# Optimization experiments

Measured on AMD Instinct MI355X. Metric: run time of the kernel, lower is better.

Reference implementation:

```python
import jax, jax.numpy as jnp
import numpy as np

N = 50000   # nodes
E = 800000  # edges
IN = 256    # input feature dim
H = 4       # heads (per layer)
D = 64      # num_hidden per head
C = 16      # n_clusters
NEG = 0.2   # leaky_relu negative slope


def _gat_conv(x, W, attn_l, attn_r, src, dst):
    """DGL GATConv (no residual, no dropout at eval), activation=elu.
    x: [N, F_in], W: [F_in, H*D], attn_l/attn_r: [H, D]. Returns [N, H, D]."""
    feat = (x @ W).reshape(N, H, D)                      # [N,H,D]
    el = jnp.sum(feat * attn_l, axis=-1)                 # [N,H]
    er = jnp.sum(feat * attn_r, axis=-1)                 # [N,H]
    e = jax.nn.leaky_relu(el[src] + er[dst], NEG)        # [E,H]
    # numerically stable segment softmax over incoming edges of each dst node
    emax = jax.ops.segment_max(e, dst, num_segments=N)   # [N,H]
    emax = jnp.where(jnp.isfinite(emax), emax, 0.0)
    ee = jnp.exp(e - emax[dst])                          # [E,H]
    denom = jax.ops.segment_sum(ee, dst, num_segments=N) # [N,H]
    a = ee / jnp.maximum(denom[dst], 1e-9)               # [E,H]
    msg = feat[src] * a[:, :, None]                      # [E,H,D]
    rst = jax.ops.segment_sum(msg, dst, num_segments=N)  # [N,H,D]
    return jax.nn.elu(rst)


def setup_inputs() -> dict:
    key = jax.random.key(0)
    ks = jax.random.split(key, 12)
    def w(k, shape, fan):
        return jax.random.normal(k, shape, jnp.float32) * np.float32(1.0 / np.sqrt(fan))
    return {
        "x": jax.random.normal(ks[0], (N, IN), jnp.float32),
        "src": jax.random.randint(ks[1], (E,), 0, N, jnp.int32),
        "dst": jax.random.randint(ks[2], (E,), 0, N, jnp.int32),
        "W0": w(ks[3], (IN, H * D), IN),
        "al0": w(ks[4], (H, D), D),
        "ar0": w(ks[5], (H, D), D),
        "W1": w(ks[6], (H * D, H * D), H * D),
        "al1": w(ks[7], (H, D), D),
        "ar1": w(ks[8], (H, D), D),
        "Wc": w(ks[9], (D, C), D),
        "bc": jnp.zeros((C,), jnp.float32),
    }


def reference(x, src, dst, W0, al0, ar0, W1, al1, ar1, Wc, bc):
    h = _gat_conv(x, W0, al0, ar0, src, dst)              # [N,H,D]
    h = _gat_conv(h.reshape(N, H * D), W1, al1, ar1, src, dst)
    heads = jnp.transpose(h, (1, 0, 2))                   # [H,N,D]
    # original bug: same cluster layer (index num_layers-1) used for every head
    cs = jax.nn.softmax(jnp.einsum("hnd,dc->hnc", heads, Wc) + bc, axis=-1)  # [H,N,C]
    # pack (heads, cs) into one array along last dim for a single output
    return jnp.concatenate([heads, cs], axis=-1)          # [H,N,D+C]
```

## Files before the change

### kernel.cpp

```cpp
#include <hip/hip_runtime.h>
#include <hip/hip_bf16.h>
#include <math.h>

#define N_NODES 50000
#define N_EDGES 800000
#define NH 4
#define ND 64
#define NF 256
#define NC 16
#define NEG_SLOPE 0.2f
#define NSLICE 4
#define SLICE_W 64

typedef __attribute__((ext_vector_type(8))) short bf16x8;
typedef __attribute__((ext_vector_type(4))) float f32x4;

__device__ __forceinline__ float elu_f(float x) {
    return x > 0.f ? x : (__expf(x) - 1.f);
}

__device__ __forceinline__ ushort bf16_rne(float f) {
    union { float f; unsigned u; } v; v.f = f;
    unsigned u = v.u;
    u += 0x7fffu + ((u >> 16) & 1u);
    return (ushort)(u >> 16);
}

__device__ __forceinline__ float bf2f(ushort u) {
    return __uint_as_float(((unsigned)u) << 16);
}

__global__ __launch_bounds__(256) void cast_bf16_kernel(const float* __restrict__ in,
                                                        ushort* __restrict__ out, int n8) {
    int i = blockIdx.x * 256 + threadIdx.x;
    if (i >= n8) return;
    float4 a = *(const float4*)(in + i * 8);
    float4 b = *(const float4*)(in + i * 8 + 4);
    ushort o[8] = {bf16_rne(a.x), bf16_rne(a.y), bf16_rne(a.z), bf16_rne(a.w),
                   bf16_rne(b.x), bf16_rne(b.y), bf16_rne(b.z), bf16_rne(b.w)};
    *(bf16x8*)(out + i * 8) = *(bf16x8*)o;
}

__global__ __launch_bounds__(256) void castWt_kernel(const float* __restrict__ W0,
                                                     const float* __restrict__ W1,
                                                     ushort* __restrict__ Wt0,
                                                     ushort* __restrict__ Wt1) {
    const float* W = (blockIdx.x < 256) ? W0 : W1;
    ushort* Wt = (blockIdx.x < 256) ? Wt0 : Wt1;
    int n = blockIdx.x & 255;
    int k = threadIdx.x;
    Wt[n * 256 + k] = bf16_rne(W[k * 256 + n]);
}

__global__ __launch_bounds__(256) void gemm_bf16(const ushort* __restrict__ A,
                                                 const ushort* __restrict__ Bt,
                                                 ushort* __restrict__ Cs,
                                                 const float* __restrict__ al,
                                                 const float* __restrict__ ar,
                                                 float* __restrict__ el,
                                                 float* __restrict__ er, int M) {
    __shared__ __align__(16) ushort As[128 * 64];
    __shared__ __align__(16) ushort Bs[128 * 64];
    const int t = threadIdx.x;
    const int l = t & 63;
    const int w = t >> 6;
    const int wm = (w >> 1) * 64, wn = (w & 1) * 64;
    const int m0 = blockIdx.x * 128, n0 = blockIdx.y * 128;
    const int lr = l & 15, lk = l >> 4;

    f32x4 acc[4][4] = {};
    const int sr = t >> 3;
    const int sc = t & 7;
    const int scw = sc ^ (sr & 7);

    for (int k0 = 0; k0 < 256; k0 += 64) {
        #pragma unroll
        for (int q = 0; q < 4; ++q) {
            int row = q * 32 + sr;
            int ga = min(m0 + row, M - 1);
            bf16x8 va = *(const bf16x8*)(A + (size_t)ga * 256 + k0 + sc * 8);
            *(bf16x8*)(&As[row * 64 + scw * 8]) = va;
            bf16x8 vb = *(const bf16x8*)(Bt + (size_t)(n0 + row) * 256 + k0 + sc * 8);
            *(bf16x8*)(&Bs[row * 64 + scw * 8]) = vb;
        }
        __syncthreads();
        #pragma unroll
        for (int kk = 0; kk < 2; ++kk) {
            bf16x8 af[4], bfr[4];
            #pragma unroll
            for (int mi = 0; mi < 4; ++mi) {
                int row = wm + mi * 16 + lr;
                int kb = kk * 4 + lk;
                af[mi] = *(const bf16x8*)(&As[row * 64 + (kb ^ (row & 7)) * 8]);
            }
            #pragma unroll
            for (int ni = 0; ni < 4; ++ni) {
                int col = wn + ni * 16 + lr;
                int kb = kk * 4 + lk;
                bfr[ni] = *(const bf16x8*)(&Bs[col * 64 + (kb ^ (col & 7)) * 8]);
            }
            #pragma unroll
            for (int mi = 0; mi < 4; ++mi)
                #pragma unroll
                for (int ni = 0; ni < 4; ++ni)
                    acc[mi][ni] = __builtin_amdgcn_mfma_f32_16x16x32_bf16(af[mi], bfr[ni], acc[mi][ni], 0, 0, 0);
        }
        __syncthreads();
    }
    const int h = (n0 + wn) >> 6;
    float alv[4], arv[4];
    #pragma unroll
    for (int ni = 0; ni < 4; ++ni) {
        alv[ni] = al[h * ND + ni * 16 + lr];
        arv[ni] = ar[h * ND + ni * 16 + lr];
    }
    #pragma unroll
    for (int mi = 0; mi < 4; ++mi) {
        #pragma unroll
        for (int j = 0; j < 4; ++j) {
            int row = m0 + wm + mi * 16 + lk * 4 + j;
            float pe = 0.f, pr = 0.f;
            #pragma unroll
            for (int ni = 0; ni < 4; ++ni) {
                int col = n0 + wn + ni * 16 + lr;
                float v = acc[mi][ni][j];
                pe += v * alv[ni];
                pr += v * arv[ni];
                if (row < M)
                    Cs[(size_t)(col >> 6) * N_NODES * SLICE_W + (size_t)row * SLICE_W + (col & 63)] = bf16_rne(v);
            }
            #pragma unroll
            for (int m = 1; m <= 8; m <<= 1) {
                pe += __shfl_xor(pe, m, 64);
                pr += __shfl_xor(pr, m, 64);
            }
            if (lr == 0 && row < M) {
                el[h * N_NODES + row] = pe;
                er[h * N_NODES + row] = pr;
            }
        }
    }
}

__global__ __launch_bounds__(256) void hist_kernel(const int* __restrict__ dst, int* __restrict__ count) {
    int e = blockIdx.x * 256 + threadIdx.x;
    if (e < N_EDGES) atomicAdd(&count[dst[e]], 1);
}

__global__ __launch_bounds__(256) void scan1_kernel(const int* __restrict__ counts,
                                                    int* __restrict__ offs,
                                                    int* __restrict__ bsums) {
    __shared__ int sh[256];
    int tid = threadIdx.x;
    int i = blockIdx.x * 256 + tid;
    int v = (i < N_NODES) ? counts[i] : 0;
    sh[tid] = v;
    __syncthreads();
    #pragma unroll
    for (int ofs = 1; ofs < 256; ofs <<= 1) {
        int t = (tid >= ofs) ? sh[tid - ofs] : 0;
        __syncthreads();
        sh[tid] += t;
        __syncthreads();
    }
    if (i < N_NODES) offs[i] = sh[tid] - v;
    if (tid == 255) bsums[blockIdx.x] = sh[255];
}

__global__ __launch_bounds__(256) void scan2_kernel(const int* __restrict__ bsums,
                                                    int* __restrict__ boffs, int nb) {
    __shared__ int sh[256];
    int tid = threadIdx.x;
    int v = (tid < nb) ? bsums[tid] : 0;
    sh[tid] = v;
    __syncthreads();
    #pragma unroll
    for (int ofs = 1; ofs < 256; ofs <<= 1) {
        int t = (tid >= ofs) ? sh[tid - ofs] : 0;
        __syncthreads();
        sh[tid] += t;
        __syncthreads();
    }
    if (tid < nb) boffs[tid] = sh[tid] - v;
}

__global__ __launch_bounds__(256) void scan3_kernel(int* __restrict__ offs,
                                                    const int* __restrict__ boffs,
                                                    int* __restrict__ cursor) {
    int i = blockIdx.x * 256 + threadIdx.x;
    if (i < N_NODES) {
        int v = offs[i] + boffs[i >> 8];
        offs[i] = v;
        cursor[i] = v;
    }
    if (i == 0) offs[N_NODES] = N_EDGES;
}

__global__ __launch_bounds__(256) void scatter_kernel(const int* __restrict__ src,
                                                      const int* __restrict__ dst,
                                                      int* __restrict__ cursor,
                                                      int* __restrict__ csrc) {
    int e = blockIdx.x * 256 + threadIdx.x;
    if (e >= N_EDGES) return;
    int p = atomicAdd(&cursor[dst[e]], 1);
    csrc[p] = src[e];
}

#define AGG9_EDGE(K)                                                                \
        int i##K = s0 + min(t + K, degc);                                           \
        int a##K = csrc[i##K];
#define AGG9_EL(K)                                                                  \
        float e##K = elh[a##K];
#define AGG9_Q(K)                                                                   \
        bf16x8 q##K = *(const bf16x8*)(basef + a##K * SLICE_W);
#define AGG9_W(K)                                                                   \
        float x##K = e##K + ern; x##K = fmaxf(x##K, NEG_SLOPE * x##K);              \
        float w##K = (t + K < deg) ? __expf(x##K) : 0.f;
#define AGG9_ACC(K)                                                                 \
        ac0 += w##K * bf2f((ushort)(q##K)[0]);                                      \
        ac1 += w##K * bf2f((ushort)(q##K)[1]);                                      \
        ac2 += w##K * bf2f((ushort)(q##K)[2]);                                      \
        ac3 += w##K * bf2f((ushort)(q##K)[3]);                                      \
        ac4 += w##K * bf2f((ushort)(q##K)[4]);                                      \
        ac5 += w##K * bf2f((ushort)(q##K)[5]);                                      \
        ac6 += w##K * bf2f((ushort)(q##K)[6]);                                      \
        ac7 += w##K * bf2f((ushort)(q##K)[7]);                                      \
        dsum += w##K;

#define AGG9_BODY()                                                                 \
    int b = blockIdx.x;                                                             \
    int slice = b & 3;                                                              \
    int wid = threadIdx.x >> 6;                                                     \
    int lane = threadIdx.x & 63;                                                    \
    int nn = lane >> 3;                                                             \
    int fc = lane & 7;                                                              \
    int h = slice;                                                                  \
    int n = (b >> 2) * 32 + wid * 8 + nn;                                           \
    int nc = min(n, N_NODES - 1);                                                   \
    const ushort* basef = fs + (size_t)slice * (N_NODES * SLICE_W) + fc * 8;        \
    const float* elh = el + (size_t)h * N_NODES;                                    \
    int s0 = offs[nc];                                                              \
    int deg = (n < N_NODES) ? (offs[nc + 1] - s0) : 0;                              \
    int degc = max(deg - 1, 0);                                                     \
    float ern = er[(size_t)h * N_NODES + nc];                                       \
    int md = deg;                                                                   \
    md = max(md, __shfl_xor(md, 8, 64));                                            \
    md = max(md, __shfl_xor(md, 16, 64));                                           \
    md = max(md, __shfl_xor(md, 32, 64));                                           \
    float ac0 = 0.f, ac1 = 0.f, ac2 = 0.f, ac3 = 0.f;                               \
    float ac4 = 0.f, ac5 = 0.f, ac6 = 0.f, ac7 = 0.f;                               \
    float dsum = 0.f;                                                               \
    for (int t = 0; t < md; t += 8) {                                               \
        AGG9_EDGE(0) AGG9_EDGE(1) AGG9_EDGE(2) AGG9_EDGE(3)                         \
        AGG9_EDGE(4) AGG9_EDGE(5) AGG9_EDGE(6) AGG9_EDGE(7)                         \
        AGG9_EL(0) AGG9_EL(1) AGG9_EL(2) AGG9_EL(3)                                 \
        AGG9_EL(4) AGG9_EL(5) AGG9_EL(6) AGG9_EL(7)                                 \
        AGG9_Q(0) AGG9_Q(1) AGG9_Q(2) AGG9_Q(3)                                     \
        AGG9_Q(4) AGG9_Q(5) AGG9_Q(6) AGG9_Q(7)                                     \
        AGG9_W(0) AGG9_W(1) AGG9_W(2) AGG9_W(3)                                     \
        AGG9_W(4) AGG9_W(5) AGG9_W(6) AGG9_W(7)                                     \
        AGG9_ACC(0) AGG9_ACC(1) AGG9_ACC(2) AGG9_ACC(3)                             \
        AGG9_ACC(4) AGG9_ACC(5) AGG9_ACC(6) AGG9_ACC(7)                             \
    }                                                                               \
    float inv = 1.f / fmaxf(dsum, 1e-9f);

__global__ __launch_bounds__(256) void agg9_l0(const ushort* __restrict__ fs,
                                               const int* __restrict__ csrc,
                                               const int* __restrict__ offs,
                                               const float* __restrict__ el,
                                               const float* __restrict__ er,
                                               ushort* __restrict__ hbuf) {
    AGG9_BODY()
    if (n < N_NODES) {
        ushort o[8] = {bf16_rne(elu_f(ac0 * inv)), bf16_rne(elu_f(ac1 * inv)),
                       bf16_rne(elu_f(ac2 * inv)), bf16_rne(elu_f(ac3 * inv)),
                       bf16_rne(elu_f(ac4 * inv)), bf16_rne(elu_f(ac5 * inv)),
                       bf16_rne(elu_f(ac6 * inv)), bf16_rne(elu_f(ac7 * inv))};
        *(bf16x8*)(hbuf + (size_t)n * NF + slice * SLICE_W + fc * 8) = *(bf16x8*)o;
    }
}

__global__ __launch_bounds__(256) void agg9_final(const ushort* __restrict__ fs,
                                                  const int* __restrict__ csrc,
                                                  const int* __restrict__ offs,
                                                  const float* __restrict__ el,
                                                  const float* __restrict__ er,
                                                  float* __restrict__ out) {
    AGG9_BODY()
    if (n < N_NODES) {
        size_t p = (size_t)h * N_NODES * (ND + NC) + (size_t)n * (ND + NC) + fc * 8;
        *(float4*)(out + p)     = make_float4(elu_f(ac0 * inv), elu_f(ac1 * inv),
                                              elu_f(ac2 * inv), elu_f(ac3 * inv));
        *(float4*)(out + p + 4) = make_float4(elu_f(ac4 * inv), elu_f(ac5 * inv),
                                              elu_f(ac6 * inv), elu_f(ac7 * inv));
    }
}

__global__ __launch_bounds__(256) void cluster_kernel(const float* __restrict__ Wc,
                                                      const float* __restrict__ bc,
                                                      float* __restrict__ out) {
    __shared__ float WcS[ND * NC];
    __shared__ float bcS[NC];
    int tid = threadIdx.x;
    #pragma unroll
    for (int i = 0; i < 4; ++i) WcS[i * 256 + tid] = Wc[i * 256 + tid];
    if (tid < NC) bcS[tid] = bc[tid];
    __syncthreads();
    int wid = tid >> 6;
    int lane = tid & 63;
    int h = lane >> 4, c = lane & 15;
    int n = blockIdx.x * 4 + wid;
    size_t base = (size_t)h * N_NODES * (ND + NC) + (size_t)n * (ND + NC);
    const float* hp = out + base;
    float acc = bcS[c];
    #pragma unroll
    for (int dd = 0; dd < 16; ++dd) {
        float4 f4 = *(const float4*)(hp + dd * 4);
        acc += f4.x * WcS[(dd * 4 + 0) * NC + c];
        acc += f4.y * WcS[(dd * 4 + 1) * NC + c];
        acc += f4.z * WcS[(dd * 4 + 2) * NC + c];
        acc += f4.w * WcS[(dd * 4 + 3) * NC + c];
    }
    float m = acc;
    m = fmaxf(m, __shfl_xor(m, 1, 64));
    m = fmaxf(m, __shfl_xor(m, 2, 64));
    m = fmaxf(m, __shfl_xor(m, 4, 64));
    m = fmaxf(m, __shfl_xor(m, 8, 64));
    float e = __expf(acc - m);
    float s = e;
    s += __shfl_xor(s, 1, 64);
    s += __shfl_xor(s, 2, 64);
    s += __shfl_xor(s, 4, 64);
    s += __shfl_xor(s, 8, 64);
    out[base + ND + c] = e / s;
}

extern "C" void kernel_launch(void* const* d_in, const int* in_sizes, int n_in,
                              void* d_out, int out_size, void* d_ws, size_t ws_size,
                              hipStream_t stream) {
    const float* x   = (const float*)d_in[0];
    const int* src   = (const int*)d_in[1];
    const int* dst   = (const int*)d_in[2];
    const float* W0  = (const float*)d_in[3];
    const float* al0 = (const float*)d_in[4];
    const float* ar0 = (const float*)d_in[5];
    const float* W1  = (const float*)d_in[6];
    const float* al1 = (const float*)d_in[7];
    const float* ar1 = (const float*)d_in[8];
    const float* Wc  = (const float*)d_in[9];
    const float* bc  = (const float*)d_in[10];
    float* out = (float*)d_out;

    char* ws = (char*)d_ws;
    size_t off = 0;
    auto alloc = [&](size_t bytes) { void* p = ws + off; off = (off + bytes + 255) & ~(size_t)255; return p; };
    ushort* featsl = (ushort*)alloc((size_t)N_NODES * NF * 2);
    ushort* xbf    = (ushort*)alloc((size_t)N_NODES * NF * 2);
    ushort* hbuf   = (ushort*)alloc((size_t)N_NODES * NF * 2);
    ushort* Wt0    = (ushort*)alloc((size_t)256 * 256 * 2);
    ushort* Wt1    = (ushort*)alloc((size_t)256 * 256 * 2);
    float*  el     = (float*)alloc((size_t)N_NODES * NH * 4);
    float*  er     = (float*)alloc((size_t)N_NODES * NH * 4);
    int* counts    = (int*)alloc((size_t)N_NODES * 4);
    int* offs      = (int*)alloc((size_t)(N_NODES + 1) * 4);
    int* cursor    = (int*)alloc((size_t)N_NODES * 4);
    int* csrc      = (int*)alloc((size_t)N_EDGES * 4);
    int* bsums     = (int*)alloc(256 * 4);
    int* boffs     = (int*)alloc(256 * 4);

    const int EB = (N_EDGES + 255) / 256;
    const int NB = (N_NODES + 255) / 256;
    const int GEMM_MB = (N_NODES + 127) / 128;
    const int C8 = (N_NODES * NF / 8 + 255) / 256;
    const int AGG_B = NSLICE * ((N_NODES + 31) / 32);

    hipMemsetAsync(counts, 0, (size_t)N_NODES * 4, stream);
    hist_kernel<<<EB, 256, 0, stream>>>(dst, counts);
    scan1_kernel<<<NB, 256, 0, stream>>>(counts, offs, bsums);
    scan2_kernel<<<1, 256, 0, stream>>>(bsums, boffs, NB);
    scan3_kernel<<<NB, 256, 0, stream>>>(offs, boffs, cursor);
    scatter_kernel<<<EB, 256, 0, stream>>>(src, dst, cursor, csrc);

    castWt_kernel<<<512, 256, 0, stream>>>(W0, W1, Wt0, Wt1);
    cast_bf16_kernel<<<C8, 256, 0, stream>>>(x, xbf, N_NODES * NF / 8);

    gemm_bf16<<<dim3(GEMM_MB, 2), 256, 0, stream>>>(xbf, Wt0, featsl, al0, ar0, el, er, N_NODES);
    agg9_l0<<<AGG_B, 256, 0, stream>>>(featsl, csrc, offs, el, er, hbuf);

    gemm_bf16<<<dim3(GEMM_MB, 2), 256, 0, stream>>>(hbuf, Wt1, featsl, al1, ar1, el, er, N_NODES);
    agg9_final<<<AGG_B, 256, 0, stream>>>(featsl, csrc, offs, el, er, out);

    cluster_kernel<<<N_NODES / 4, 256, 0, stream>>>(Wc, bc, out);
}
```

Measured before the change: 307.0 us.

## Widen feature slices to two heads per slice and pre-scale logits by log2e

Measured after the change: 319.1 us. 1.04x slower.

```diff
diff --git a/kernel.cpp b/kernel.cpp
--- a/kernel.cpp
+++ b/kernel.cpp
@@ -9,8 +9,9 @@
 #define NF 256
 #define NC 16
 #define NEG_SLOPE 0.2f
-#define NSLICE 4
-#define SLICE_W 64
+#define NSLICE 2
+#define SLICE_W 128
+#define LOG2E 1.44269504088896340736f
 
 typedef __attribute__((ext_vector_type(8))) short bf16x8;
 typedef __attribute__((ext_vector_type(4))) float f32x4;
@@ -127,7 +128,7 @@
                 pe += v * alv[ni];
                 pr += v * arv[ni];
                 if (row < M)
-                    Cs[(size_t)(col >> 6) * N_NODES * SLICE_W + (size_t)row * SLICE_W + (col & 63)] = bf16_rne(v);
+                    Cs[(size_t)(col >> 7) * N_NODES * SLICE_W + (size_t)row * SLICE_W + (col & 127)] = bf16_rne(v);
             }
             #pragma unroll
             for (int m = 1; m <= 8; m <<= 1) {
@@ -135,8 +136,8 @@
                 pr += __shfl_xor(pr, m, 64);
             }
             if (lr == 0 && row < M) {
-                el[h * N_NODES + row] = pe;
-                er[h * N_NODES + row] = pr;
+                el[h * N_NODES + row] = pe * LOG2E;
+                er[h * N_NODES + row] = pr * LOG2E;
             }
         }
     }
@@ -206,38 +207,47 @@
     csrc[p] = src[e];
 }
 
-#define AGG9_EDGE(K)                                                                \
+#define AGG10_E(K)                                                                  \
         int i##K = s0 + min(t + K, degc);                                           \
         int a##K = csrc[i##K];
-#define AGG9_EL(K)                                                                  \
+#define AGG10_EL(K)                                                                 \
         float e##K = elh[a##K];
-#define AGG9_Q(K)                                                                   \
-        bf16x8 q##K = *(const bf16x8*)(basef + a##K * SLICE_W);
-#define AGG9_W(K)                                                                   \
+#define AGG10_Q(K)                                                                  \
+        bf16x8 qa##K = *(const bf16x8*)(basef + a##K * SLICE_W);                    \
+        bf16x8 qb##K = *(const bf16x8*)(basef + a##K * SLICE_W + 8);
+#define AGG10_W(K)                                                                  \
         float x##K = e##K + ern; x##K = fmaxf(x##K, NEG_SLOPE * x##K);              \
-        float w##K = (t + K < deg) ? __expf(x##K) : 0.f;
-#define AGG9_ACC(K)                                                                 \
-        ac0 += w##K * bf2f((ushort)(q##K)[0]);                                      \
-        ac1 += w##K * bf2f((ushort)(q##K)[1]);                                      \
-        ac2 += w##K * bf2f((ushort)(q##K)[2]);                                      \
-        ac3 += w##K * bf2f((ushort)(q##K)[3]);                                      \
-        ac4 += w##K * bf2f((ushort)(q##K)[4]);                                      \
-        ac5 += w##K * bf2f((ushort)(q##K)[5]);                                      \
-        ac6 += w##K * bf2f((ushort)(q##K)[6]);                                      \
-        ac7 += w##K * bf2f((ushort)(q##K)[7]);                                      \
+        float w##K = (t + K < deg) ? exp2f(x##K) : 0.f;
+#define AGG10_ACC(K)                                                                \
+        ac0 += w##K * bf2f((ushort)(qa##K)[0]);                                     \
+        ac1 += w##K * bf2f((ushort)(qa##K)[1]);                                     \
+        ac2 += w##K * bf2f((ushort)(qa##K)[2]);                                     \
+        ac3 += w##K * bf2f((ushort)(qa##K)[3]);                                     \
+        ac4 += w##K * bf2f((ushort)(qa##K)[4]);                                     \
+        ac5 += w##K * bf2f((ushort)(qa##K)[5]);                                     \
+        ac6 += w##K * bf2f((ushort)(qa##K)[6]);                                     \
+        ac7 += w##K * bf2f((ushort)(qa##K)[7]);                                     \
+        ac8  += w##K * bf2f((ushort)(qb##K)[0]);                                    \
+        ac9  += w##K * bf2f((ushort)(qb##K)[1]);                                    \
+        ac10 += w##K * bf2f((ushort)(qb##K)[2]);                                    \
+        ac11 += w##K * bf2f((ushort)(qb##K)[3]);                                    \
+        ac12 += w##K * bf2f((ushort)(qb##K)[4]);                                    \
+        ac13 += w##K * bf2f((ushort)(qb##K)[5]);                                    \
+        ac14 += w##K * bf2f((ushort)(qb##K)[6]);                                    \
+        ac15 += w##K * bf2f((ushort)(qb##K)[7]);                                    \
         dsum += w##K;
 
-#define AGG9_BODY()                                                                 \
+#define AGG10_BODY()                                                                \
     int b = blockIdx.x;                                                             \
-    int slice = b & 3;                                                              \
+    int slice = b & 1;                                                              \
     int wid = threadIdx.x >> 6;                                                     \
     int lane = threadIdx.x & 63;                                                    \
     int nn = lane >> 3;                                                             \
     int fc = lane & 7;                                                              \
-    int h = slice;                                                                  \
-    int n = (b >> 2) * 32 + wid * 8 + nn;                                           \
+    int h = slice * 2 + (fc >> 2);                                                  \
+    int n = (b >> 1) * 32 + wid * 8 + nn;                                           \
     int nc = min(n, N_NODES - 1);                                                   \
-    const ushort* basef = fs + (size_t)slice * (N_NODES * SLICE_W) + fc * 8;        \
+    const ushort* basef = fs + (size_t)slice * (N_NODES * SLICE_W) + fc * 16;       \
     const float* elh = el + (size_t)h * N_NODES;                                    \
     int s0 = offs[nc];                                                              \
     int deg = (n < N_NODES) ? (offs[nc + 1] - s0) : 0;                              \
@@ -249,50 +259,58 @@
     md = max(md, __shfl_xor(md, 32, 64));                                           \
     float ac0 = 0.f, ac1 = 0.f, ac2 = 0.f, ac3 = 0.f;                               \
     float ac4 = 0.f, ac5 = 0.f, ac6 = 0.f, ac7 = 0.f;                               \
+    float ac8 = 0.f, ac9 = 0.f, ac10 = 0.f, ac11 = 0.f;                             \
+    float ac12 = 0.f, ac13 = 0.f, ac14 = 0.f, ac15 = 0.f;                           \
     float dsum = 0.f;                                                               \
-    for (int t = 0; t < md; t += 8) {                                               \
-        AGG9_EDGE(0) AGG9_EDGE(1) AGG9_EDGE(2) AGG9_EDGE(3)                         \
-        AGG9_EDGE(4) AGG9_EDGE(5) AGG9_EDGE(6) AGG9_EDGE(7)                         \
-        AGG9_EL(0) AGG9_EL(1) AGG9_EL(2) AGG9_EL(3)                                 \
-        AGG9_EL(4) AGG9_EL(5) AGG9_EL(6) AGG9_EL(7)                                 \
-        AGG9_Q(0) AGG9_Q(1) AGG9_Q(2) AGG9_Q(3)                                     \
-        AGG9_Q(4) AGG9_Q(5) AGG9_Q(6) AGG9_Q(7)                                     \
-        AGG9_W(0) AGG9_W(1) AGG9_W(2) AGG9_W(3)                                     \
-        AGG9_W(4) AGG9_W(5) AGG9_W(6) AGG9_W(7)                                     \
-        AGG9_ACC(0) AGG9_ACC(1) AGG9_ACC(2) AGG9_ACC(3)                             \
-        AGG9_ACC(4) AGG9_ACC(5) AGG9_ACC(6) AGG9_ACC(7)                             \
+    for (int t = 0; t < md; t += 4) {                                               \
+        AGG10_E(0) AGG10_E(1) AGG10_E(2) AGG10_E(3)                                 \
+        AGG10_EL(0) AGG10_EL(1) AGG10_EL(2) AGG10_EL(3)                             \
+        AGG10_Q(0) AGG10_Q(1) AGG10_Q(2) AGG10_Q(3)                                 \
+        AGG10_W(0) AGG10_W(1) AGG10_W(2) AGG10_W(3)                                 \
+        AGG10_ACC(0) AGG10_ACC(1) AGG10_ACC(2) AGG10_ACC(3)                         \
     }                                                                               \
     float inv = 1.f / fmaxf(dsum, 1e-9f);
 
-__global__ __launch_bounds__(256) void agg9_l0(const ushort* __restrict__ fs,
-                                               const int* __restrict__ csrc,
-                                               const int* __restrict__ offs,
-                                               const float* __restrict__ el,
-                                               const float* __restrict__ er,
-                                               ushort* __restrict__ hbuf) {
-    AGG9_BODY()
+__global__ __launch_bounds__(256) void agg10_l0(const ushort* __restrict__ fs,
+                                                const int* __restrict__ csrc,
+                                                const int* __restrict__ offs,
+                                                const float* __restrict__ el,
+                                                const float* __restrict__ er,
+                                                ushort* __restrict__ hbuf) {
+    AGG10_BODY()
     if (n < N_NODES) {
-        ushort o[8] = {bf16_rne(elu_f(ac0 * inv)), bf16_rne(elu_f(ac1 * inv)),
-                       bf16_rne(elu_f(ac2 * inv)), bf16_rne(elu_f(ac3 * inv)),
-                       bf16_rne(elu_f(ac4 * inv)), bf16_rne(elu_f(ac5 * inv)),
-                       bf16_rne(elu_f(ac6 * inv)), bf16_rne(elu_f(ac7 * inv))};
-        *(bf16x8*)(hbuf + (size_t)n * NF + slice * SLICE_W + fc * 8) = *(bf16x8*)o;
-    }
-}
-
-__global__ __launch_bounds__(256) void agg9_final(const ushort* __restrict__ fs,
-                                                  const int* __restrict__ csrc,
-                                                  const int* __restrict__ offs,
-                                                  const float* __restrict__ el,
-                                                  const float* __restrict__ er,
-                                                  float* __restrict__ out) {
-    AGG9_BODY()
+        ushort oa[8] = {bf16_rne(elu_f(ac0 * inv)), bf16_rne(elu_f(ac1 * inv)),
+                        bf16_rne(elu_f(ac2 * inv)), bf16_rne(elu_f(ac3 * inv)),
+                        bf16_rne(elu_f(ac4 * inv)), bf16_rne(elu_f(ac5 * inv)),
+                        bf16_rne(elu_f(ac6 * inv)), bf16_rne(elu_f(ac7 * inv))};
+        ushort ob[8] = {bf16_rne(elu_f(ac8 * inv)),  bf16_rne(elu_f(ac9 * inv)),
+                        bf16_rne(elu_f(ac10 * inv)), bf16_rne(elu_f(ac11 * inv)),
+                        bf16_rne(elu_f(ac12 * inv)), bf16_rne(elu_f(ac13 * inv)),
+                        bf16_rne(elu_f(ac14 * inv)), bf16_rne(elu_f(ac15 * inv))};
+        ushort* p = hbuf + (size_t)n * NF + slice * SLICE_W + fc * 16;
+        *(bf16x8*)(p)     = *(bf16x8*)oa;
+        *(bf16x8*)(p + 8) = *(bf16x8*)ob;
+    }
+}
+
+__global__ __launch_bounds__(256) void agg10_final(const ushort* __restrict__ fs,
+                                                   const int* __restrict__ csrc,
+                                                   const int* __restrict__ offs,
+                                                   const float* __restrict__ el,
+                                                   const float* __restrict__ er,
+                                                   float* __restrict__ out) {
+    AGG10_BODY()
     if (n < N_NODES) {
-        size_t p = (size_t)h * N_NODES * (ND + NC) + (size_t)n * (ND + NC) + fc * 8;
-        *(float4*)(out + p)     = make_float4(elu_f(ac0 * inv), elu_f(ac1 * inv),
-                                              elu_f(ac2 * inv), elu_f(ac3 * inv));
-        *(float4*)(out + p + 4) = make_float4(elu_f(ac4 * inv), elu_f(ac5 * inv),
-                                              elu_f(ac6 * inv), elu_f(ac7 * inv));
+        int d0 = (fc & 3) * 16;
+        size_t p = (size_t)h * N_NODES * (ND + NC) + (size_t)n * (ND + NC) + d0;
+        *(float4*)(out + p)      = make_float4(elu_f(ac0 * inv),  elu_f(ac1 * inv),
+                                               elu_f(ac2 * inv),  elu_f(ac3 * inv));
+        *(float4*)(out + p + 4)  = make_float4(elu_f(ac4 * inv),  elu_f(ac5 * inv),
+                                               elu_f(ac6 * inv),  elu_f(ac7 * inv));
+        *(float4*)(out + p + 8)  = make_float4(elu_f(ac8 * inv),  elu_f(ac9 * inv),
+                                               elu_f(ac10 * inv), elu_f(ac11 * inv));
+        *(float4*)(out + p + 12) = make_float4(elu_f(ac12 * inv), elu_f(ac13 * inv),
+                                               elu_f(ac14 * inv), elu_f(ac15 * inv));
     }
 }
 
@@ -385,10 +403,10 @@
     cast_bf16_kernel<<<C8, 256, 0, stream>>>(x, xbf, N_NODES * NF / 8);
 
     gemm_bf16<<<dim3(GEMM_MB, 2), 256, 0, stream>>>(xbf, Wt0, featsl, al0, ar0, el, er, N_NODES);
-    agg9_l0<<<AGG_B, 256, 0, stream>>>(featsl, csrc, offs, el, er, hbuf);
+    agg10_l0<<<AGG_B, 256, 0, stream>>>(featsl, csrc, offs, el, er, hbuf);
 
     gemm_bf16<<<dim3(GEMM_MB, 2), 256, 0, stream>>>(hbuf, Wt1, featsl, al1, ar1, el, er, N_NODES);
-    agg9_final<<<AGG_B, 256, 0, stream>>>(featsl, csrc, offs, el, er, out);
+    agg10_final<<<AGG_B, 256, 0, stream>>>(featsl, csrc, offs, el, er, out);
 
     cluster_kernel<<<N_NODES / 4, 256, 0, stream>>>(Wc, bc, out);
 }
```
